# Kernel tuning notes

Measured on AMD Instinct MI355X. Metric: run time of the kernel, lower is better.

Reference implementation:

```python
import jax, jax.numpy as jnp
from jax import lax
import numpy as np

B, T, U, V = 4, 300, 64, 1024
FEAT, H, L = 80, 512, 3            # encoder: 3-layer bidirectional LSTM
HD = 512                           # decoder hidden (1 layer)
ENC_OUT = DEC_OUT = 512
INNER = 512
DMAX = max(FEAT, 2 * H)            # padded input dim for stacked encoder weights
NEG = -1e30


def setup_inputs() -> dict:
    key = jax.random.key(0)
    ks = jax.random.split(key, 20)
    s = 1.0 / np.sqrt(H)
    u = lambda k, shp: jax.random.uniform(k, shp, jnp.float32, -s, s)
    inputs = jax.random.normal(ks[0], (B, T, FEAT), jnp.float32)
    inputs_length = jax.random.randint(ks[1], (B,), T // 2, T + 1, jnp.int32)
    targets = jax.random.randint(ks[2], (B, U), 1, V, jnp.int32)
    targets_length = jax.random.randint(ks[3], (B,), U // 2, U + 1, jnp.int32)
    enc_Wih = u(ks[4], (L, 2, 4 * H, DMAX))   # layer0 uses first FEAT cols
    enc_Whh = u(ks[5], (L, 2, 4 * H, H))
    enc_b = u(ks[6], (L, 2, 4 * H))           # b_ih + b_hh fused
    enc_proj_W = u(ks[7], (ENC_OUT, 2 * H))
    enc_proj_b = u(ks[8], (ENC_OUT,))
    dec_emb = u(ks[9], (V, HD)).at[0].set(0.0)  # padding_idx=0
    dec_Wih = u(ks[10], (4 * HD, HD))
    dec_Whh = u(ks[11], (4 * HD, HD))
    dec_b = u(ks[12], (4 * HD,))
    dec_proj_W = u(ks[13], (DEC_OUT, HD))
    dec_proj_b = u(ks[14], (DEC_OUT,))
    j_fwd_W = u(ks[15], (INNER, ENC_OUT + DEC_OUT))
    j_fwd_b = u(ks[16], (INNER,))
    j_proj_W = u(ks[17], (V, INNER))
    j_proj_b = u(ks[18], (V,))
    return dict(inputs=inputs, inputs_length=inputs_length, targets=targets,
                targets_length=targets_length, enc_Wih=enc_Wih, enc_Whh=enc_Whh,
                enc_b=enc_b, enc_proj_W=enc_proj_W, enc_proj_b=enc_proj_b,
                dec_emb=dec_emb, dec_Wih=dec_Wih, dec_Whh=dec_Whh, dec_b=dec_b,
                dec_proj_W=dec_proj_W, dec_proj_b=dec_proj_b, j_fwd_W=j_fwd_W,
                j_fwd_b=j_fwd_b, j_proj_W=j_proj_W, j_proj_b=j_proj_b)


def lstm_layer(x, Wih, Whh, b):
    # x: [B, T, Din]; torch gate order (i, f, g, o)
    Bb = x.shape[0]
    Hh = Whh.shape[1]
    xg = jnp.einsum('btd,gd->btg', x, Wih) + b  # precompute input projections

    def step(carry, xt):
        h, c = carry
        g = xt + h @ Whh.T
        i, f, gg, o = jnp.split(g, 4, axis=-1)
        c = jax.nn.sigmoid(f) * c + jax.nn.sigmoid(i) * jnp.tanh(gg)
        h = jax.nn.sigmoid(o) * jnp.tanh(c)
        return (h, c), h

    z = jnp.zeros((Bb, Hh), x.dtype)
    _, hs = lax.scan(step, (z, z), xg.transpose(1, 0, 2))
    return hs.transpose(1, 0, 2)


def reverse_padded(x, lengths):
    # reverse each sequence within its valid length (packed-sequence semantics)
    t = jnp.arange(x.shape[1])
    idx = jnp.where(t[None] < lengths[:, None], lengths[:, None] - 1 - t[None], t[None])
    return jnp.take_along_axis(x, idx[:, :, None], axis=1)


def rnnt_loss(log_probs, targets, T_len, U_len):
    # log_probs: [B, T, U+1, V], blank = 0
    Bb, Tt, U1, _ = log_probs.shape
    Uu = U1 - 1
    blank = log_probs[..., 0]                                   # [B,T,U+1]
    idx = jnp.broadcast_to(targets[:, None, :, None], (Bb, Tt, Uu, 1))
    lab = jnp.take_along_axis(log_probs[:, :, :Uu, :], idx, axis=3)[..., 0]  # [B,T,U]

    def row_update(a, c):
        # solves x[u] = logaddexp(a[u], x[u-1] + c[u-1]) via log-space cumsum
        C = jnp.concatenate([jnp.zeros((Bb, 1), a.dtype), jnp.cumsum(c, axis=1)], axis=1)
        return C + lax.cumlogsumexp(a - C, axis=1)

    a0 = jnp.full((Bb, U1), NEG, log_probs.dtype).at[:, 0].set(0.0)
    alpha0 = row_update(a0, lab[:, 0])

    def step(alpha_prev, xs):
        bl_prev, lab_t = xs
        alpha = row_update(alpha_prev + bl_prev, lab_t)
        return alpha, alpha

    xs = (blank[:, :-1].transpose(1, 0, 2), lab[:, 1:].transpose(1, 0, 2))
    _, alphas = lax.scan(step, alpha0, xs)                      # [T-1,B,U+1]
    alphas = jnp.concatenate([alpha0[None], alphas], axis=0)    # [T,B,U+1]
    b_idx = jnp.arange(Bb)
    ll = alphas[T_len - 1, b_idx, U_len] + blank[b_idx, T_len - 1, U_len]
    return -jnp.mean(ll)


def reference(inputs, inputs_length, targets, targets_length, enc_Wih, enc_Whh,
              enc_b, enc_proj_W, enc_proj_b, dec_emb, dec_Wih, dec_Whh, dec_b,
              dec_proj_W, dec_proj_b, j_fwd_W, j_fwd_b, j_proj_W, j_proj_b):
    # ---- encoder: stacked bi-LSTM + projection ----
    mask = (jnp.arange(T)[None] < inputs_length[:, None])[..., None].astype(inputs.dtype)
    x = inputs
    for l in range(L):
        Din = x.shape[-1]
        fwd = lstm_layer(x, enc_Wih[l, 0, :, :Din], enc_Whh[l, 0], enc_b[l, 0])
        bwd = reverse_padded(
            lstm_layer(reverse_padded(x, inputs_length), enc_Wih[l, 1, :, :Din],
                       enc_Whh[l, 1], enc_b[l, 1]), inputs_length)
        x = jnp.concatenate([fwd, bwd], axis=-1) * mask
    enc = jnp.einsum('bth,oh->bto', x, enc_proj_W) + enc_proj_b  # [B,T,ENC_OUT]

    # ---- decoder: blank-prepended targets -> embed -> LSTM -> projection ----
    dec_in = jnp.pad(targets, ((0, 0), (1, 0)))                  # [B,U+1]
    demb = dec_emb[dec_in]
    dmask = (jnp.arange(U + 1)[None] < (targets_length + 1)[:, None])[..., None].astype(demb.dtype)
    dh = lstm_layer(demb, dec_Wih, dec_Whh, dec_b) * dmask
    dec = jnp.einsum('buh,oh->buo', dh, dec_proj_W) + dec_proj_b  # [B,U+1,DEC_OUT]

    # ---- joint: broadcast T x (U+1), split concat-matmul into two matmuls ----
    We, Wd = j_fwd_W[:, :ENC_OUT], j_fwd_W[:, ENC_OUT:]
    hj = jnp.tanh(jnp.einsum('bto,io->bti', enc, We)[:, :, None, :]
                  + jnp.einsum('buo,io->bui', dec, Wd)[:, None, :, :] + j_fwd_b)
    logits = jnp.einsum('btui,vi->btuv', hj, j_proj_W) + j_proj_b  # [B,T,U+1,V]
    log_probs = jax.nn.log_softmax(logits, axis=-1)

    return rnnt_loss(log_probs, targets, inputs_length, targets_length)
```

## Files before the change

kernel.cpp:

```cpp
#include <hip/hip_runtime.h>
#include <hip/hip_bf16.h>

#define B_ 4
#define T_ 300
#define U_ 64
#define U1_ 65
#define V_ 1024
#define H_ 512
#define G4_ 2048
#define NW_ 32
#define RPB_ (T_ * U1_)
#define NTILE_ 305
#define RPAD_ 19520

typedef __hip_bfloat16 bf16;
typedef unsigned long long u64;
typedef __attribute__((ext_vector_type(8))) short short8;
typedef __attribute__((ext_vector_type(4))) float floatx4;

__device__ __forceinline__ float b2f(bf16 x) { return __bfloat162float(x); }
__device__ __forceinline__ bf16 f2b(float x) { return __float2bfloat16(x); }
__device__ __forceinline__ short bf16bits(float x) {
  bf16 h = __float2bfloat16(x);
  return *reinterpret_cast<short*>(&h);
}
__device__ __forceinline__ short8 pack8(float4 a, float4 b) {
  short8 p;
  p[0] = bf16bits(a.x); p[1] = bf16bits(a.y); p[2] = bf16bits(a.z); p[3] = bf16bits(a.w);
  p[4] = bf16bits(b.x); p[5] = bf16bits(b.y); p[6] = bf16bits(b.z); p[7] = bf16bits(b.w);
  return p;
}
__device__ __forceinline__ float sigm_(float x) { return 1.f / (1.f + __expf(-x)); }
__device__ __forceinline__ float tanh_(float x) { return 1.f - 2.f / (1.f + __expf(2.f * x)); }
__device__ __forceinline__ float lae_(float x, float y) {
  float m = fmaxf(x, y);
  float n = fminf(x, y);
  return m + __logf(1.f + __expf(n - m));
}

__global__ void prep_kernel(const float* __restrict__ in, bf16* __restrict__ x0) {
  int i = blockIdx.x * 256 + threadIdx.x;
  if (i < B_ * T_ * 128) {
    int k = i & 127;
    int row = i >> 7;
    float v = (k < 80) ? in[row * 80 + k] : 0.f;
    x0[(size_t)row * 1024 + k] = f2b(v);
  }
}

__global__ void embed_kernel(const float* __restrict__ emb, const int* __restrict__ tgt,
                             bf16* __restrict__ demb) {
  int i = blockIdx.x * 256 + threadIdx.x;
  if (i >= B_ * U1_ * 512) return;
  int k = i & 511;
  int bu = i >> 9;
  int u = bu % U1_, b = bu / U1_;
  int id = (u == 0) ? 0 : tgt[b * U_ + u - 1];
  demb[i] = f2b(emb[(size_t)id * 512 + k]);
}

__global__ __launch_bounds__(256) void gemm_kernel(
    const bf16* __restrict__ A, int lda,
    const float* __restrict__ W, int ldw,
    const float* __restrict__ bias,
    void* __restrict__ Cout, int out_f32, int ldc,
    int M, int K) {
  __shared__ __align__(16) bf16 As[64][72];
  __shared__ __align__(16) bf16 Bs[64][72];
  int m0 = blockIdx.x * 64, n0 = blockIdx.y * 64;
  int tid = threadIdx.x, w = tid >> 6, l = tid & 63;
  int l4 = l & 15, lq = l >> 4;
  floatx4 acc[4];
#pragma unroll
  for (int nt = 0; nt < 4; ++nt) acc[nt] = (floatx4){0.f, 0.f, 0.f, 0.f};
  for (int k0 = 0; k0 < K; k0 += 64) {
    __syncthreads();
#pragma unroll
    for (int q = 0; q < 2; ++q) {
      int cc = tid + q * 256;
      int r = cc >> 3, kc = (cc & 7) * 8;
      short8 va = {0, 0, 0, 0, 0, 0, 0, 0};
      int gm = m0 + r;
      if (gm < M) va = *(const short8*)(A + (size_t)gm * lda + k0 + kc);
      *(short8*)(&As[r][kc]) = va;
      const float* wp = W + (size_t)(n0 + r) * ldw + k0 + kc;
      float4 w0 = *(const float4*)(wp);
      float4 w1 = *(const float4*)(wp + 4);
      *(short8*)(&Bs[r][kc]) = pack8(w0, w1);
    }
    __syncthreads();
#pragma unroll
    for (int kk = 0; kk < 64; kk += 32) {
      short8 a = *(const short8*)(&As[w * 16 + l4][kk + lq * 8]);
#pragma unroll
      for (int nt = 0; nt < 4; ++nt) {
        short8 bb = *(const short8*)(&Bs[nt * 16 + l4][kk + lq * 8]);
        acc[nt] = __builtin_amdgcn_mfma_f32_16x16x32_bf16(a, bb, acc[nt], 0, 0, 0);
      }
    }
  }
#pragma unroll
  for (int nt = 0; nt < 4; ++nt) {
    int col = n0 + nt * 16 + l4;
    float bv = bias ? bias[col] : 0.f;
#pragma unroll
    for (int r = 0; r < 4; ++r) {
      int row = m0 + w * 16 + lq * 4 + r;
      if (row < M) {
        float v = acc[nt][r] + bv;
        if (out_f32) ((float*)Cout)[(size_t)row * ldc + col] = v;
        else ((bf16*)Cout)[(size_t)row * ldc + col] = f2b(v);
      }
    }
  }
}

__global__ __launch_bounds__(256, 1) void scan_kernel(
    const float* __restrict__ xg,
    const float* __restrict__ whh,
    const int* __restrict__ len_raw, int len_add,
    int Tmax, int bwd_mask,
    bf16* __restrict__ out, int out_stride,
    int dec_d,
    const float* __restrict__ xg2, const float* __restrict__ whh2,
    const int* __restrict__ len_raw2, int len_add2,
    int Tmax2, bf16* __restrict__ out2, int out_stride2,
    u64* __restrict__ hpk) {
  int w = blockIdx.x, d = blockIdx.y;
  int tid = threadIdx.x;
  bool isdec = (d == dec_d);
  const float* xg_d = isdec ? xg2 : xg + (size_t)d * B_ * Tmax * G4_;
  const float* whh_d = isdec ? whh2 : whh + (size_t)d * G4_ * H_;
  const int* lens = isdec ? len_raw2 : len_raw;
  int ladd = isdec ? len_add2 : len_add;
  int tmax = isdec ? Tmax2 : Tmax;
  bf16* outp = isdec ? out2 : out;
  int ostride = isdec ? out_stride2 : out_stride;
  int ocol = isdec ? 0 : d * H_;
  bool bwd = isdec ? false : ((bwd_mask >> d) & 1);
  u64* hp = hpk + (size_t)d * 4096;

  int row = tid & 63;
  int ks = tid >> 6;
  int lane = row;
  int grow = (row >> 4) * H_ + w * 16 + (row & 15);

  float wreg[128];
  {
    const float* wp = whh_d + (size_t)grow * H_ + ks * 128;
#pragma unroll
    for (int j = 0; j < 128; ++j) wreg[j] = wp[j];
  }

  __shared__ __align__(16) float h_lds[4][512];
  __shared__ float partialT[2][4][4][68];
  __shared__ float xvsT[2][4][68];
  __shared__ float c_lds[16][4];
  __shared__ int len_s[4];

  if (tid < 4) len_s[tid] = lens[tid] + ladd;
  if (tid < 64) c_lds[tid & 15][tid >> 4] = 0.f;
  __syncthreads();
  int smax = max(max(len_s[0], len_s[1]), max(len_s[2], len_s[3]));

  int d0 = ks * 128 + lane;
  int d1 = d0 + 64;

  for (int s = 0; s < smax; ++s) {
    int p = s & 1;
    bool ract = s < len_s[ks];
    int rt = bwd ? (len_s[ks] - 1 - s) : s;
    if (!ract) rt = 0;
    float xv = xg_d[((size_t)ks * tmax + rt) * G4_ + grow];

    if (s == 0) {
#pragma unroll
      for (int b = 0; b < 4; ++b) { h_lds[b][d0] = 0.f; h_lds[b][d1] = 0.f; }
    } else {
      const u64* src = hp + ((s - 1) & 1) * 2048;
      u64 v[8];
      for (;;) {
        bool ok = true;
#pragma unroll
        for (int b = 0; b < 4; ++b) {
          v[2 * b] = __hip_atomic_load(src + b * 512 + d0, __ATOMIC_RELAXED,
                                       __HIP_MEMORY_SCOPE_AGENT);
          v[2 * b + 1] = __hip_atomic_load(src + b * 512 + d1, __ATOMIC_RELAXED,
                                           __HIP_MEMORY_SCOPE_AGENT);
          ok &= ((int)(unsigned)v[2 * b] == s) & ((int)(unsigned)v[2 * b + 1] == s);
        }
        if (__all(ok)) break;
      }
#pragma unroll
      for (int b = 0; b < 4; ++b) {
        h_lds[b][d0] = __uint_as_float((unsigned)(v[2 * b] >> 32));
        h_lds[b][d1] = __uint_as_float((unsigned)(v[2 * b + 1] >> 32));
      }
    }
    xvsT[p][ks][row] = xv;
    float a0 = 0.f, a1 = 0.f, a2 = 0.f, a3 = 0.f;
    {
      int kb = ks * 128;
      const float4* hb0 = (const float4*)&h_lds[0][kb];
      const float4* hb1 = (const float4*)&h_lds[1][kb];
      const float4* hb2 = (const float4*)&h_lds[2][kb];
      const float4* hb3 = (const float4*)&h_lds[3][kb];
#pragma unroll
      for (int j = 0; j < 32; ++j) {
        float w0 = wreg[4 * j], w1 = wreg[4 * j + 1], w2 = wreg[4 * j + 2], w3 = wreg[4 * j + 3];
        float4 x0 = hb0[j], x1 = hb1[j], x2 = hb2[j], x3 = hb3[j];
        a0 += w0 * x0.x + w1 * x0.y + w2 * x0.z + w3 * x0.w;
        a1 += w0 * x1.x + w1 * x1.y + w2 * x1.z + w3 * x1.w;
        a2 += w0 * x2.x + w1 * x2.y + w2 * x2.z + w3 * x2.w;
        a3 += w0 * x3.x + w1 * x3.y + w2 * x3.z + w3 * x3.w;
      }
    }
    partialT[p][0][ks][row] = a0;
    partialT[p][1][ks][row] = a1;
    partialT[p][2][ks][row] = a2;
    partialT[p][3][ks][row] = a3;
    __syncthreads();
    if (tid < 64) {
      int dim = tid & 15, bb = tid >> 4;
      float g[4];
#pragma unroll
      for (int gg = 0; gg < 4; ++gg) {
        int r = gg * 16 + dim;
        g[gg] = partialT[p][bb][0][r] + partialT[p][bb][1][r] +
                partialT[p][bb][2][r] + partialT[p][bb][3][r] + xvsT[p][bb][r];
      }
      bool wactive = s < len_s[bb];
      float hval = 0.f;
      if (wactive) {
        float c = c_lds[dim][bb];
        c = sigm_(g[1]) * c + sigm_(g[0]) * tanh_(g[2]);
        hval = sigm_(g[3]) * tanh_(c);
        c_lds[dim][bb] = c;
      }
      u64 pkt = ((u64)__float_as_uint(hval) << 32) | (unsigned)(s + 1);
      __hip_atomic_store(hp + p * 2048 + bb * 512 + w * 16 + dim, pkt,
                         __ATOMIC_RELAXED, __HIP_MEMORY_SCOPE_AGENT);
      if (wactive) {
        int t = bwd ? (len_s[bb] - 1 - s) : s;
        outp[((size_t)bb * tmax + t) * ostride + ocol + w * 16 + dim] = f2b(hval);
      }
    }
  }
}

__global__ __launch_bounds__(256) void joint_kernel(
    const float* __restrict__ ea, const float* __restrict__ da,
    const float* __restrict__ Wp, const float* __restrict__ pb,
    const int* __restrict__ targets,
    float* __restrict__ blankraw, float* __restrict__ labraw,
    float* __restrict__ jstats) {
  __shared__ __align__(16) bf16 As[64][72];
  __shared__ __align__(16) bf16 Bs[256][72];
  __shared__ float bias_s[256];
  __shared__ int tgt_s[64];
  __shared__ float pstat[64][2][2];

  int tid = threadIdx.x;
  int tile = blockIdx.x, cb = blockIdx.y, b = blockIdx.z;
  int r0 = tile * 64;

  bias_s[tid & 255] = pb[cb * 256 + (tid & 255)];
  if (tid < 64) {
    int r = r0 + tid;
    int u = r % U1_;
    tgt_s[tid] = (r < RPB_ && u < U_) ? targets[b * U_ + u] : -1;
  }
  int si = tid >> 2;
  int sseg = (tid & 3) * 16;
  int sr = r0 + si;
  bool svalid = sr < RPB_;
  int st = svalid ? sr / U1_ : 0;
  int su = svalid ? sr % U1_ : 0;
  const float* ep = ea + ((size_t)(b * T_ + st)) * 512 + sseg;
  const float* dp = da + ((size_t)(b * U1_ + su)) * 512 + sseg;

  int wid = tid >> 6, l = tid & 63;
  int wm = wid >> 1, wn = wid & 1;
  int l4 = l & 15, lq = l >> 4;

  floatx4 acc[2][8];
#pragma unroll
  for (int ms = 0; ms < 2; ++ms)
#pragma unroll
    for (int nt = 0; nt < 8; ++nt) acc[ms][nt] = (floatx4){0.f, 0.f, 0.f, 0.f};

  for (int k0 = 0; k0 < 512; k0 += 64) {
    __syncthreads();
    {
      const float* e = ep + k0;
      const float* d = dp + k0;
#pragma unroll
      for (int h = 0; h < 2; ++h) {
        float4 e0 = *(const float4*)(e + h * 8);
        float4 e1 = *(const float4*)(e + h * 8 + 4);
        float4 d0 = *(const float4*)(d + h * 8);
        float4 d1 = *(const float4*)(d + h * 8 + 4);
        short8 pk = {0, 0, 0, 0, 0, 0, 0, 0};
        if (svalid) {
          pk[0] = bf16bits(tanh_(e0.x + d0.x));
          pk[1] = bf16bits(tanh_(e0.y + d0.y));
          pk[2] = bf16bits(tanh_(e0.z + d0.z));
          pk[3] = bf16bits(tanh_(e0.w + d0.w));
          pk[4] = bf16bits(tanh_(e1.x + d1.x));
          pk[5] = bf16bits(tanh_(e1.y + d1.y));
          pk[6] = bf16bits(tanh_(e1.z + d1.z));
          pk[7] = bf16bits(tanh_(e1.w + d1.w));
        }
        *(short8*)(&As[si][sseg + h * 8]) = pk;
      }
    }
#pragma unroll
    for (int q = 0; q < 8; ++q) {
      int cc = tid + q * 256;
      int r = cc >> 3, kc = (cc & 7) * 8;
      const float* wp = Wp + (size_t)(cb * 256 + r) * 512 + k0 + kc;
      float4 w0 = *(const float4*)(wp);
      float4 w1 = *(const float4*)(wp + 4);
      *(short8*)(&Bs[r][kc]) = pack8(w0, w1);
    }
    __syncthreads();
#pragma unroll
    for (int kk = 0; kk < 64; kk += 32) {
      short8 af[2], bf8[8];
#pragma unroll
      for (int ms = 0; ms < 2; ++ms)
        af[ms] = *(const short8*)(&As[wm * 32 + ms * 16 + l4][kk + lq * 8]);
#pragma unroll
      for (int nt = 0; nt < 8; ++nt)
        bf8[nt] = *(const short8*)(&Bs[wn * 128 + nt * 16 + l4][kk + lq * 8]);
#pragma unroll
      for (int ms = 0; ms < 2; ++ms)
#pragma unroll
        for (int nt = 0; nt < 8; ++nt)
          acc[ms][nt] = __builtin_amdgcn_mfma_f32_16x16x32_bf16(af[ms], bf8[nt], acc[ms][nt], 0, 0, 0);
    }
  }
#pragma unroll
  for (int ms = 0; ms < 2; ++ms) {
#pragma unroll
    for (int r = 0; r < 4; ++r) {
      int i = wm * 32 + ms * 16 + lq * 4 + r;
      int grow = r0 + i;
      bool valid = grow < RPB_;
      int tg = tgt_s[i];
      float v[8];
      float mx = -1e30f;
#pragma unroll
      for (int nt = 0; nt < 8; ++nt) {
        int colc = wn * 128 + nt * 16 + l4;
        float x = acc[ms][nt][r] + bias_s[colc];
        v[nt] = x;
        mx = fmaxf(mx, x);
        int gcol = cb * 256 + colc;
        if (valid) {
          if (gcol == 0) blankraw[(size_t)b * RPB_ + grow] = x;
          if (gcol == tg) labraw[(size_t)b * RPB_ + grow] = x;
        }
      }
#pragma unroll
      for (int dd = 1; dd < 16; dd <<= 1) mx = fmaxf(mx, __shfl_xor(mx, dd, 64));
      float se = 0.f;
#pragma unroll
      for (int nt = 0; nt < 8; ++nt) se += __expf(v[nt] - mx);
#pragma unroll
      for (int dd = 1; dd < 16; dd <<= 1) se += __shfl_xor(se, dd, 64);
      if (l4 == 0) { pstat[i][wn][0] = mx; pstat[i][wn][1] = se; }
    }
  }
  __syncthreads();
  if (tid < 64) {
    float ma = pstat[tid][0][0], sa = pstat[tid][0][1];
    float mb = pstat[tid][1][0], sb = pstat[tid][1][1];
    float mc = fmaxf(ma, mb);
    float sc = sa * __expf(ma - mc) + sb * __expf(mb - mc);
    size_t o = (((size_t)b * RPAD_ + r0 + tid) * 4 + cb) * 2;
    jstats[o] = mc;
    jstats[o + 1] = sc;
  }
}

__global__ void finalize_kernel(const float* __restrict__ jstats,
                                float* __restrict__ blank, float* __restrict__ lab) {
  int g = blockIdx.x * 256 + threadIdx.x;
  if (g >= B_ * RPB_) return;
  int b = g / RPB_, r = g % RPB_;
  const float* st = jstats + ((size_t)b * RPAD_ + r) * 8;
  float M = fmaxf(fmaxf(st[0], st[2]), fmaxf(st[4], st[6]));
  float s = st[1] * __expf(st[0] - M) + st[3] * __expf(st[2] - M) +
            st[5] * __expf(st[4] - M) + st[7] * __expf(st[6] - M);
  float lse = M + __logf(s);
  blank[g] -= lse;
  if ((r % U1_) < U_) lab[g] -= lse;
}

__global__ void loss_kernel(const float* __restrict__ blank, const float* __restrict__ lab,
                            const int* __restrict__ Tl, const int* __restrict__ Ul,
                            float* __restrict__ outp) {
  int b = threadIdx.x >> 6;
  int l = threadIdx.x & 63;
  int TL = Tl[b], UL = Ul[b];
  float alpha_l = 0.f, alpha0 = 0.f;
  for (int t = 0; t < TL; ++t) {
    float a_u0, a_l1;
    if (t == 0) { a_u0 = 0.f; a_l1 = -1e30f; }
    else {
      const float* bl = blank + ((size_t)b * T_ + (t - 1)) * U1_;
      a_u0 = alpha0 + bl[0];
      a_l1 = alpha_l + bl[l + 1];
    }
    const float* lb = lab + ((size_t)b * T_ + t) * U1_;
    float C = lb[l];
#pragma unroll
    for (int dd = 1; dd < 64; dd <<= 1) {
      float o = __shfl_up(C, dd, 64);
      if (l >= dd) C += o;
    }
    float S = a_l1 - C;
#pragma unroll
    for (int dd = 1; dd < 64; dd <<= 1) {
      float o = __shfl_up(S, dd, 64);
      if (l >= dd) S = lae_(S, o);
    }
    alpha_l = C + lae_(a_u0, S);
    alpha0 = a_u0;
  }
  float av = (UL == 0) ? alpha0 : __shfl(alpha_l, UL - 1, 64);
  float ll = av + blank[((size_t)b * T_ + (TL - 1)) * U1_ + UL];
  __shared__ float lls[4];
  if (l == 0) lls[b] = ll;
  __syncthreads();
  if (threadIdx.x == 0) outp[0] = -0.25f * (lls[0] + lls[1] + lls[2] + lls[3]);
}

static constexpr size_t OFF_XG = 0;
static constexpr size_t OFF_XA = OFF_XG + (size_t)2 * B_ * T_ * G4_ * 4;
static constexpr size_t OFF_XB = OFF_XA + (size_t)B_ * T_ * 1024 * 2;
static constexpr size_t OFF_ENC = OFF_XB + (size_t)B_ * T_ * 1024 * 2;
static constexpr size_t OFF_EA = OFF_ENC + (size_t)B_ * T_ * 512 * 2;
static constexpr size_t OFF_DEMB = OFF_EA + (size_t)B_ * T_ * 512 * 4;
static constexpr size_t OFF_DXG = OFF_DEMB + (size_t)B_ * U1_ * 512 * 2;
static constexpr size_t OFF_DH = OFF_DXG + (size_t)B_ * U1_ * G4_ * 4;
static constexpr size_t OFF_DEC = OFF_DH + (size_t)B_ * U1_ * 512 * 2;
static constexpr size_t OFF_DA = OFF_DEC + (size_t)B_ * U1_ * 512 * 2;
static constexpr size_t OFF_BL = OFF_DA + (size_t)B_ * U1_ * 512 * 4;
static constexpr size_t OFF_LAB = OFF_BL + (size_t)B_ * T_ * U1_ * 4;
static constexpr size_t OFF_HPK = OFF_LAB + (size_t)B_ * T_ * U1_ * 4;
static constexpr size_t OFF_JST = OFF_HPK + (size_t)7 * 4096 * 8;

extern "C" void kernel_launch(void* const* d_in, const int* in_sizes, int n_in,
                              void* d_out, int out_size, void* d_ws, size_t ws_size,
                              hipStream_t stream) {
  (void)in_sizes; (void)n_in; (void)out_size; (void)ws_size;
  const float* inputs = (const float*)d_in[0];
  const int* inputs_length = (const int*)d_in[1];
  const int* targets = (const int*)d_in[2];
  const int* targets_length = (const int*)d_in[3];
  const float* enc_Wih = (const float*)d_in[4];
  const float* enc_Whh = (const float*)d_in[5];
  const float* enc_b = (const float*)d_in[6];
  const float* enc_proj_W = (const float*)d_in[7];
  const float* enc_proj_b = (const float*)d_in[8];
  const float* dec_emb = (const float*)d_in[9];
  const float* dec_Wih = (const float*)d_in[10];
  const float* dec_Whh = (const float*)d_in[11];
  const float* dec_b = (const float*)d_in[12];
  const float* dec_proj_W = (const float*)d_in[13];
  const float* dec_proj_b = (const float*)d_in[14];
  const float* j_fwd_W = (const float*)d_in[15];
  const float* j_fwd_b = (const float*)d_in[16];
  const float* j_proj_W = (const float*)d_in[17];
  const float* j_proj_b = (const float*)d_in[18];

  char* ws = (char*)d_ws;
  float* xg = (float*)(ws + OFF_XG);
  bf16* xa = (bf16*)(ws + OFF_XA);
  bf16* xb = (bf16*)(ws + OFF_XB);
  bf16* encb = (bf16*)(ws + OFF_ENC);
  float* eab = (float*)(ws + OFF_EA);
  bf16* demb = (bf16*)(ws + OFF_DEMB);
  float* dxg = (float*)(ws + OFF_DXG);
  bf16* dh = (bf16*)(ws + OFF_DH);
  bf16* decb = (bf16*)(ws + OFF_DEC);
  float* dab = (float*)(ws + OFF_DA);
  float* blank = (float*)(ws + OFF_BL);
  float* lab = (float*)(ws + OFF_LAB);
  u64* hpk = (u64*)(ws + OFF_HPK);
  float* jstats = (float*)(ws + OFF_JST);

  prep_kernel<<<600, 256, 0, stream>>>(inputs, xa);
  embed_kernel<<<520, 256, 0, stream>>>(dec_emb, targets, demb);

  gemm_kernel<<<dim3(5, 32), 256, 0, stream>>>(demb, 512, dec_Wih, 512, dec_b,
                                               dxg, 1, G4_, B_ * U1_, 512);
  for (int dd = 0; dd < 2; ++dd) {
    gemm_kernel<<<dim3(19, 32), 256, 0, stream>>>(
        xa, 1024, enc_Wih + (size_t)dd * G4_ * 1024, 1024, enc_b + (size_t)dd * G4_,
        xg + (size_t)dd * B_ * T_ * G4_, 1, G4_, B_ * T_, 128);
  }
  scan_kernel<<<dim3(NW_, 3), 256, 0, stream>>>(
      xg, enc_Whh, inputs_length, 0, T_, 2, xb, 1024,
      2, dxg, dec_Whh, targets_length, 1, U1_, dh, 512,
      hpk);

  gemm_kernel<<<dim3(5, 8), 256, 0, stream>>>(dh, 512, dec_proj_W, 512, dec_proj_b,
                                              decb, 0, 512, B_ * U1_, 512);
  gemm_kernel<<<dim3(5, 8), 256, 0, stream>>>(decb, 512, j_fwd_W + 512, 1024, j_fwd_b,
                                              dab, 1, 512, B_ * U1_, 512);

  bf16* xcur = xb;
  for (int lyr = 1; lyr < 3; ++lyr) {
    bf16* xnext = (xcur == xa) ? xb : xa;
    for (int dd = 0; dd < 2; ++dd) {
      gemm_kernel<<<dim3(19, 32), 256, 0, stream>>>(
          xcur, 1024,
          enc_Wih + (size_t)(lyr * 2 + dd) * G4_ * 1024, 1024,
          enc_b + (size_t)(lyr * 2 + dd) * G4_,
          xg + (size_t)dd * B_ * T_ * G4_, 1, G4_, B_ * T_, 1024);
    }
    scan_kernel<<<dim3(NW_, 2), 256, 0, stream>>>(
        xg, enc_Whh + (size_t)lyr * 2 * G4_ * H_,
        inputs_length, 0, T_, 2, xnext, 1024,
        -1, dxg, dec_Whh, targets_length, 1, U1_, dh, 512,
        hpk + (size_t)(3 + 2 * (lyr - 1)) * 4096);
    xcur = xnext;
  }
  gemm_kernel<<<dim3(19, 8), 256, 0, stream>>>(xcur, 1024, enc_proj_W, 1024, enc_proj_b,
                                               encb, 0, 512, B_ * T_, 1024);
  gemm_kernel<<<dim3(19, 8), 256, 0, stream>>>(encb, 512, j_fwd_W, 1024, (const float*)nullptr,
                                               eab, 1, 512, B_ * T_, 512);

  joint_kernel<<<dim3(NTILE_, 4, B_), 256, 0, stream>>>(eab, dab, j_proj_W, j_proj_b, targets,
                                                        blank, lab, jstats);
  finalize_kernel<<<(B_ * RPB_ + 255) / 256, 256, 0, stream>>>(jstats, blank, lab);
  loss_kernel<<<1, 256, 0, stream>>>(blank, lab, inputs_length, targets_length, (float*)d_out);
}
```

Baseline: 4.122 ms.

## Compute LSTM recurrent matvec with bf16 MFMA and split hi/lo hidden state

The per-step recurrent product h·Whh^T moves from scalar fp32 FMAs over register-held weights to `mfma_f32_16x16x32_bf16`, with weights packed to bf16 in registers. The hidden state is stored in swizzled LDS as bf16 high plus bf16 residual rows, so the MFMA rows sum to a near-fp32 h. The thread-to-work mapping changes so each wave covers 4 hidden dims across all 4 gates. Gate values are combined with cross-lane shuffles instead of an LDS partial-sum reduction and a second barrier. The goal is to cut per-timestep latency in this serial chain, at the cost of rounding Whh to bf16.

```diff
diff --git a/kernel.cpp b/kernel.cpp
--- a/kernel.cpp
+++ b/kernel.cpp
@@ -140,109 +140,118 @@
   bool bwd = isdec ? false : ((bwd_mask >> d) & 1);
   u64* hp = hpk + (size_t)d * 4096;
 
-  int row = tid & 63;
-  int ks = tid >> 6;
-  int lane = row;
-  int grow = (row >> 4) * H_ + w * 16 + (row & 15);
-
-  float wreg[128];
+  int sub = tid >> 6;
+  int l = tid & 63;
+  int col = l & 15;
+  int lq = l >> 4;
+  int gate = col & 3;
+  int dloc = col >> 2;
+  int dim = w * 16 + sub * 4 + dloc;
+  int grow = gate * H_ + dim;
+  int sb = l & 12;
+
+  __shared__ int len_s[4];
+  __shared__ __align__(16) bf16 h_lds[2][16][512];
+
+  if (tid < 4) len_s[tid] = lens[tid] + ladd;
   {
-    const float* wp = whh_d + (size_t)grow * H_ + ks * 128;
-#pragma unroll
-    for (int j = 0; j < 128; ++j) wreg[j] = wp[j];
-  }
-
-  __shared__ __align__(16) float h_lds[4][512];
-  __shared__ float partialT[2][4][4][68];
-  __shared__ float xvsT[2][4][68];
-  __shared__ float c_lds[16][4];
-  __shared__ int len_s[4];
-
-  if (tid < 4) len_s[tid] = lens[tid] + ladd;
-  if (tid < 64) c_lds[tid & 15][tid >> 4] = 0.f;
+    unsigned* hz = (unsigned*)&h_lds[0][0][0];
+#pragma unroll
+    for (int i = 0; i < 32; ++i) hz[tid + i * 256] = 0u;
+  }
+
+  short8 bfr[16];
+  {
+    const float* wp = whh_d + (size_t)grow * H_ + lq * 8;
+#pragma unroll
+    for (int ks2 = 0; ks2 < 16; ++ks2) {
+      float4 w0 = *(const float4*)(wp + ks2 * 32);
+      float4 w1 = *(const float4*)(wp + ks2 * 32 + 4);
+      bfr[ks2] = pack8(w0, w1);
+    }
+  }
   __syncthreads();
   int smax = max(max(len_s[0], len_s[1]), max(len_s[2], len_s[3]));
 
-  int d0 = ks * 128 + lane;
-  int d1 = d0 + 64;
+  int D0 = sub * 128 + 2 * l;
+  float cst = 0.f;
+  char* hbase = (char*)&h_lds[0][0][0];
+  unsigned rsw = (unsigned)((l & 7) << 4);
+  unsigned rbyte = (unsigned)((l & 15) * 1024 + lq * 16);
 
   for (int s = 0; s < smax; ++s) {
     int p = s & 1;
-    bool ract = s < len_s[ks];
-    int rt = bwd ? (len_s[ks] - 1 - s) : s;
-    if (!ract) rt = 0;
-    float xv = xg_d[((size_t)ks * tmax + rt) * G4_ + grow];
-
-    if (s == 0) {
-#pragma unroll
-      for (int b = 0; b < 4; ++b) { h_lds[b][d0] = 0.f; h_lds[b][d1] = 0.f; }
-    } else {
+    char* pl = hbase + p * 16384;
+    float xv[4];
+    if (l < 16) {
+#pragma unroll
+      for (int b = 0; b < 4; ++b) {
+        int lb = len_s[b];
+        int rt = bwd ? (lb - 1 - s) : s;
+        if (s >= lb) rt = 0;
+        xv[b] = xg_d[((size_t)b * tmax + rt) * G4_ + grow];
+      }
+    }
+    if (s > 0) {
       const u64* src = hp + ((s - 1) & 1) * 2048;
       u64 v[8];
       for (;;) {
         bool ok = true;
 #pragma unroll
         for (int b = 0; b < 4; ++b) {
-          v[2 * b] = __hip_atomic_load(src + b * 512 + d0, __ATOMIC_RELAXED,
+          v[2 * b] = __hip_atomic_load(src + b * 512 + D0, __ATOMIC_RELAXED,
                                        __HIP_MEMORY_SCOPE_AGENT);
-          v[2 * b + 1] = __hip_atomic_load(src + b * 512 + d1, __ATOMIC_RELAXED,
+          v[2 * b + 1] = __hip_atomic_load(src + b * 512 + D0 + 1, __ATOMIC_RELAXED,
                                            __HIP_MEMORY_SCOPE_AGENT);
           ok &= ((int)(unsigned)v[2 * b] == s) & ((int)(unsigned)v[2 * b + 1] == s);
         }
         if (__all(ok)) break;
       }
+      unsigned cb = (unsigned)(D0 * 2);
 #pragma unroll
       for (int b = 0; b < 4; ++b) {
-        h_lds[b][d0] = __uint_as_float((unsigned)(v[2 * b] >> 32));
-        h_lds[b][d1] = __uint_as_float((unsigned)(v[2 * b + 1] >> 32));
-      }
-    }
-    xvsT[p][ks][row] = xv;
-    float a0 = 0.f, a1 = 0.f, a2 = 0.f, a3 = 0.f;
-    {
-      int kb = ks * 128;
-      const float4* hb0 = (const float4*)&h_lds[0][kb];
-      const float4* hb1 = (const float4*)&h_lds[1][kb];
-      const float4* hb2 = (const float4*)&h_lds[2][kb];
-      const float4* hb3 = (const float4*)&h_lds[3][kb];
-#pragma unroll
-      for (int j = 0; j < 32; ++j) {
-        float w0 = wreg[4 * j], w1 = wreg[4 * j + 1], w2 = wreg[4 * j + 2], w3 = wreg[4 * j + 3];
-        float4 x0 = hb0[j], x1 = hb1[j], x2 = hb2[j], x3 = hb3[j];
-        a0 += w0 * x0.x + w1 * x0.y + w2 * x0.z + w3 * x0.w;
-        a1 += w0 * x1.x + w1 * x1.y + w2 * x1.z + w3 * x1.w;
-        a2 += w0 * x2.x + w1 * x2.y + w2 * x2.z + w3 * x2.w;
-        a3 += w0 * x3.x + w1 * x3.y + w2 * x3.z + w3 * x3.w;
-      }
-    }
-    partialT[p][0][ks][row] = a0;
-    partialT[p][1][ks][row] = a1;
-    partialT[p][2][ks][row] = a2;
-    partialT[p][3][ks][row] = a3;
+        float f0 = __uint_as_float((unsigned)(v[2 * b] >> 32));
+        float f1 = __uint_as_float((unsigned)(v[2 * b + 1] >> 32));
+        bf16 h0 = f2b(f0), h1 = f2b(f1);
+        float r0 = f0 - b2f(h0), r1 = f1 - b2f(h1);
+        bf16 e0 = f2b(r0), e1 = f2b(r1);
+        unsigned hi = (unsigned)*(unsigned short*)&h0 |
+                      ((unsigned)*(unsigned short*)&h1 << 16);
+        unsigned lo = (unsigned)*(unsigned short*)&e0 |
+                      ((unsigned)*(unsigned short*)&e1 << 16);
+        *(unsigned*)(pl + (((unsigned)(b * 1024) + cb) ^ (unsigned)(b << 4))) = hi;
+        *(unsigned*)(pl + (((unsigned)((b + 4) * 1024) + cb) ^ (unsigned)((b + 4) << 4))) = lo;
+      }
+    }
     __syncthreads();
-    if (tid < 64) {
-      int dim = tid & 15, bb = tid >> 4;
-      float g[4];
-#pragma unroll
-      for (int gg = 0; gg < 4; ++gg) {
-        int r = gg * 16 + dim;
-        g[gg] = partialT[p][bb][0][r] + partialT[p][bb][1][r] +
-                partialT[p][bb][2][r] + partialT[p][bb][3][r] + xvsT[p][bb][r];
-      }
-      bool wactive = s < len_s[bb];
-      float hval = 0.f;
-      if (wactive) {
-        float c = c_lds[dim][bb];
-        c = sigm_(g[1]) * c + sigm_(g[0]) * tanh_(g[2]);
-        hval = sigm_(g[3]) * tanh_(c);
-        c_lds[dim][bb] = c;
-      }
-      u64 pkt = ((u64)__float_as_uint(hval) << 32) | (unsigned)(s + 1);
-      __hip_atomic_store(hp + p * 2048 + bb * 512 + w * 16 + dim, pkt,
+    floatx4 acc = (floatx4){0.f, 0.f, 0.f, 0.f};
+#pragma unroll
+    for (int ks2 = 0; ks2 < 16; ++ks2) {
+      short8 a = *(const short8*)(pl + ((rbyte + (unsigned)(ks2 * 64)) ^ rsw));
+      acc = __builtin_amdgcn_mfma_f32_16x16x32_bf16(a, bfr[ks2], acc, 0, 0, 0);
+    }
+    float hout = 0.f;
+#pragma unroll
+    for (int r = 0; r < 4; ++r) {
+      float v2 = acc[r] + __shfl(acc[r], col + 16, 64);
+      if (l < 16) v2 += xv[r];
+      float gi = __shfl(v2, sb + 0, 64);
+      float gf = __shfl(v2, sb + 1, 64);
+      float gg = __shfl(v2, sb + 2, 64);
+      float go = __shfl(v2, sb + 3, 64);
+      if (l < 16 && (l & 3) == r && s < len_s[r]) {
+        cst = sigm_(gf) * cst + sigm_(gi) * tanh_(gg);
+        hout = sigm_(go) * tanh_(cst);
+      }
+    }
+    if (l < 16) {
+      int b = l & 3;
+      u64 pkt = ((u64)__float_as_uint(hout) << 32) | (unsigned)(s + 1);
+      __hip_atomic_store(hp + p * 2048 + b * 512 + dim, pkt,
                          __ATOMIC_RELAXED, __HIP_MEMORY_SCOPE_AGENT);
-      if (wactive) {
-        int t = bwd ? (len_s[bb] - 1 - s) : s;
-        outp[((size_t)bb * tmax + t) * ostride + ocol + w * 16 + dim] = f2b(hval);
+      if (s < len_s[b]) {
+        int t = bwd ? (len_s[b] - 1 - s) : s;
+        outp[((size_t)b * tmax + t) * ostride + ocol + dim] = f2b(hout);
       }
     }
   }
```

Result: faster. 3.512 ms (-14.8%).
